# Kernel tuning notes

Measured on AMD Instinct MI355X. Metric: run time of the kernel, lower is better.

Reference implementation:

```python
import jax, jax.numpy as jnp
import numpy as np

N_HEAD = 16
SCALE = True


def setup_inputs() -> dict:
    key = jax.random.key(0)
    k1, k2, k3 = jax.random.split(key, 3)
    B, S, D = 4, 2048, 1024
    x = jax.random.normal(k1, (B, S, D), dtype=jnp.float32)
    w_attn = jax.random.normal(k2, (D, 3 * D), dtype=jnp.float32) * 0.02
    b_attn = jnp.zeros((3 * D,), dtype=jnp.float32)
    w_proj = jax.random.normal(k3, (D, D), dtype=jnp.float32) * 0.02
    b_proj = jnp.zeros((D,), dtype=jnp.float32)
    return {"x": x, "w_attn": w_attn, "b_attn": b_attn, "w_proj": w_proj, "b_proj": b_proj}


def reference(x, w_attn, b_attn, w_proj, b_proj):
    B, S, D = x.shape
    H = N_HEAD
    hd = D // H
    qkv = x @ w_attn + b_attn  # [B,S,3D] (Conv1D)
    q, k, v = jnp.split(qkv, 3, axis=-1)
    # split heads -> [B,H,S,hd]
    q = q.reshape(B, S, H, hd).transpose(0, 2, 1, 3)
    k = k.reshape(B, S, H, hd).transpose(0, 2, 1, 3)
    v = v.reshape(B, S, H, hd).transpose(0, 2, 1, 3)
    w = jnp.einsum('bhqd,bhkd->bhqk', q, k)  # [B,H,S,S]
    if SCALE:
        w = w / jnp.sqrt(jnp.asarray(hd, dtype=w.dtype))
    # causal mask exactly as in source: w*b + -10000*(1-b)
    bmask = jnp.tril(jnp.ones((S, S), dtype=w.dtype))[None, None]
    w = w * bmask + (-10000.0) * (1.0 - bmask)
    w = jax.nn.softmax(w, axis=-1)
    a = jnp.einsum('bhqk,bhkd->bhqd', w, v)  # [B,H,S,hd]
    a = a.transpose(0, 2, 1, 3).reshape(B, S, D)  # merge heads
    out = a @ w_proj + b_proj
    return out
```

## Files before the change

kernel.cpp:

```cpp
#include <hip/hip_runtime.h>

typedef __attribute__((ext_vector_type(8))) _Float16 f16x8;
typedef __attribute__((ext_vector_type(2))) __fp16 h16x2;
typedef __attribute__((ext_vector_type(4))) float f32x4;

#define S_LEN 2048
#define DMODEL 1024
#define NHEAD 16
#define HD 64
#define QKV_LD 3072
#define BTOT 4
#define LOG2E 1.4426950408889634f

#define GLL16(g, l)                                              \
  __builtin_amdgcn_global_load_lds(                              \
      (const __attribute__((address_space(1))) void*)(g),        \
      (__attribute__((address_space(3))) void*)(l), 16, 0, 0)

#define MFMA16(a, b, c) __builtin_amdgcn_mfma_f32_16x16x32_f16(a, b, c, 0, 0, 0)

__global__ __launch_bounds__(256) void cvt_f32_f16_k(const float* __restrict__ in,
                                                     _Float16* __restrict__ out, int n) {
  int i = (blockIdx.x * 256 + threadIdx.x) * 4;
  int stride = gridDim.x * 256 * 4;
  for (; i < n; i += stride) {
    float4 v = *(const float4*)(in + i);
    _Float16 h[4];
    h[0] = (_Float16)v.x; h[1] = (_Float16)v.y; h[2] = (_Float16)v.z; h[3] = (_Float16)v.w;
    *(uint2*)(out + i) = *(const uint2*)h;
  }
}

__global__ __launch_bounds__(256) void transpose_cvt_k(const float* __restrict__ W,
                                                       _Float16* __restrict__ Wt,
                                                       int K, int N) {
  __shared__ float t[32][33];
  int n0 = blockIdx.x * 32, k0 = blockIdx.y * 32;
  int tx = threadIdx.x, ty = threadIdx.y;
#pragma unroll
  for (int i = 0; i < 32; i += 8)
    t[ty + i][tx] = W[(size_t)(k0 + ty + i) * N + n0 + tx];
  __syncthreads();
#pragma unroll
  for (int i = 0; i < 32; i += 8)
    Wt[(size_t)(n0 + ty + i) * K + k0 + tx] = (_Float16)t[tx][ty + i];
}

template <int OUT_F32>
__global__ __launch_bounds__(256) void gemm_bt_k(const _Float16* __restrict__ A,
                                                 const _Float16* __restrict__ Bt,
                                                 const float* __restrict__ bias,
                                                 void* __restrict__ C,
                                                 int M, int N, int K) {
  __shared__ _Float16 As[128 * 64];
  __shared__ _Float16 Bs[128 * 64];
  const int tid = threadIdx.x;
  const int wid = tid >> 6, lane = tid & 63;
  const int quad = lane >> 4, l16 = lane & 15;
  const int wr = wid >> 1, wc = wid & 1;

  const int lin = blockIdx.y * gridDim.x + blockIdx.x;
  const int width = 8 * gridDim.x;
  const int group = lin / width;
  const int pm = group * 8 + (lin % width) % 8;
  const int pn = (lin % width) / 8;
  const int tm = pm * 128, tn = pn * 128;

  const int row0 = tid >> 3;
  const int xc = 8 * ((tid & 7) ^ (row0 & 7));
  const _Float16* Ag = A + (size_t)(tm + row0) * K + xc;
  const _Float16* Bg = Bt + (size_t)(tn + row0) * K + xc;
  _Float16* AsW = &As[wid * 512];
  _Float16* BsW = &Bs[wid * 512];

  f32x4 acc[4][4] = {};

  for (int k0 = 0; k0 < K; k0 += 64) {
    __syncthreads();
#pragma unroll
    for (int p = 0; p < 4; p++) {
      GLL16(Ag + k0 + (size_t)(32 * p) * K, AsW + 2048 * p);
      GLL16(Bg + k0 + (size_t)(32 * p) * K, BsW + 2048 * p);
    }
    __syncthreads();

#pragma unroll
    for (int ks = 0; ks < 2; ks++) {
      f16x8 af[4], bf[4];
#pragma unroll
      for (int mt = 0; mt < 4; mt++)
        af[mt] = *(const f16x8*)&As[(wr * 64 + mt * 16 + l16) * 64 +
                                    (((ks * 4 + quad) ^ (l16 & 7)) << 3)];
#pragma unroll
      for (int nt = 0; nt < 4; nt++)
        bf[nt] = *(const f16x8*)&Bs[(wc * 64 + nt * 16 + l16) * 64 +
                                    (((ks * 4 + quad) ^ (l16 & 7)) << 3)];
#pragma unroll
      for (int mt = 0; mt < 4; mt++)
#pragma unroll
        for (int nt = 0; nt < 4; nt++)
          acc[mt][nt] = MFMA16(af[mt], bf[nt], acc[mt][nt]);
    }
  }

#pragma unroll
  for (int nt = 0; nt < 4; nt++) {
    int col = tn + wc * 64 + nt * 16 + l16;
    float bv = bias[col];
#pragma unroll
    for (int mt = 0; mt < 4; mt++) {
      int row = tm + wr * 64 + mt * 16 + quad * 4;
#pragma unroll
      for (int r = 0; r < 4; r++) {
        float v = acc[mt][nt][r] + bv;
        if (OUT_F32)
          ((float*)C)[(size_t)(row + r) * N + col] = v;
        else
          ((_Float16*)C)[(size_t)(row + r) * N + col] = (_Float16)v;
      }
    }
  }
}

__global__ __launch_bounds__(512, 2) void gemm256_k(const _Float16* __restrict__ A,
                                                    const _Float16* __restrict__ Bt,
                                                    const float* __restrict__ bias,
                                                    _Float16* __restrict__ C,
                                                    int M, int N, int K) {
  __shared__ __align__(16) _Float16 sb[2][2][16384];
  const int tid = threadIdx.x;
  const int wid = tid >> 6, lane = tid & 63;
  const int quad = lane >> 4, l16 = lane & 15;
  const int wm = wid >> 2, wn = wid & 3;

  const int lin = blockIdx.y * gridDim.x + blockIdx.x;
  const int width = 8 * gridDim.x;
  const int group = lin / width;
  const int pm = group * 8 + (lin % width) % 8;
  const int pn = (lin % width) / 8;
  const int tm = pm * 256, tn = pn * 256;

  const int row0 = tid >> 3;
  const int xc = 8 * ((tid & 7) ^ (row0 & 7));
  const _Float16* Ag = A + (size_t)(tm + row0) * K + xc;
  const _Float16* Bg = Bt + (size_t)(tn + row0) * K + xc;

  f32x4 acc[8][4] = {};
  const int ntk = K >> 6;

  auto stage = [&](int t) {
    const int d = t & 1;
    const int k0 = t << 6;
#pragma unroll
    for (int r = 0; r < 4; r++) {
      GLL16(Ag + k0 + (size_t)(64 * r) * K, &sb[d][0][r * 4096 + wid * 512]);
      GLL16(Bg + k0 + (size_t)(64 * r) * K, &sb[d][1][r * 4096 + wid * 512]);
    }
  };

  stage(0);
  if (ntk > 1) stage(1);

  for (int t = 0; t < ntk; t++) {
    if (t + 1 < ntk)
      asm volatile("s_waitcnt vmcnt(8)" ::: "memory");
    else
      asm volatile("s_waitcnt vmcnt(0)" ::: "memory");
    __builtin_amdgcn_s_barrier();
    asm volatile("" ::: "memory");
    __builtin_amdgcn_sched_barrier(0);

    const _Float16* As_ = sb[t & 1][0];
    const _Float16* Bs_ = sb[t & 1][1];
    f16x8 bf[4][2];
#pragma unroll
    for (int n = 0; n < 4; n++)
#pragma unroll
      for (int ks = 0; ks < 2; ks++)
        bf[n][ks] = *(const f16x8*)&Bs_[(wn * 64 + n * 16 + l16) * 64 +
                                        (((ks * 4 + quad) ^ (l16 & 7)) << 3)];
#pragma unroll
    for (int mh = 0; mh < 2; mh++) {
      f16x8 af[4][2];
#pragma unroll
      for (int m = 0; m < 4; m++)
#pragma unroll
        for (int ks = 0; ks < 2; ks++)
          af[m][ks] =
              *(const f16x8*)&As_[(wm * 128 + mh * 64 + m * 16 + l16) * 64 +
                                  (((ks * 4 + quad) ^ (l16 & 7)) << 3)];
      __builtin_amdgcn_s_setprio(1);
#pragma unroll
      for (int ks = 0; ks < 2; ks++)
#pragma unroll
        for (int m = 0; m < 4; m++)
#pragma unroll
          for (int n = 0; n < 4; n++)
            acc[mh * 4 + m][n] = MFMA16(af[m][ks], bf[n][ks], acc[mh * 4 + m][n]);
      __builtin_amdgcn_s_setprio(0);
    }

    __builtin_amdgcn_s_barrier();
    asm volatile("" ::: "memory");
    __builtin_amdgcn_sched_barrier(0);
    if (t + 2 < ntk) stage(t + 2);
  }

#pragma unroll
  for (int n = 0; n < 4; n++) {
    int col = tn + wn * 64 + n * 16 + l16;
    float bv = bias[col];
#pragma unroll
    for (int m8 = 0; m8 < 8; m8++) {
      int row = tm + wm * 128 + m8 * 16 + quad * 4;
#pragma unroll
      for (int r = 0; r < 4; r++)
        C[(size_t)(row + r) * N + col] = (_Float16)(acc[m8][n][r] + bv);
    }
  }
}

__global__ __launch_bounds__(512, 4) void attn_k(const _Float16* __restrict__ qkv,
                                                 _Float16* __restrict__ out) {
  __shared__ __align__(16) char pool[53760];
  _Float16* KsB = (_Float16*)pool;
  _Float16* VTsB = (_Float16*)(pool + 16384);

  const int tid = threadIdx.x, wid = tid >> 6, lane = tid & 63;
  const int quad = lane >> 4, l16 = lane & 15;
  const int qg = wid & 3, kg = wid >> 2;
  _Float16* PsW = (_Float16*)(pool + 32768) + wid * 1280;
  const int bh = blockIdx.x, b = bh >> 4, h = bh & 15;
  const int p = blockIdx.y;
  const _Float16* base = qkv + (size_t)b * S_LEN * QKV_LD + h * HD;

  const int krow = tid >> 3;
  const _Float16* Kg = base + DMODEL + (size_t)krow * QKV_LD +
                       8 * ((tid & 7) ^ (krow & 7));
  const bool vstager = (tid < 256);
  const int kp = tid & 31, dbase = ((tid >> 5) & 7) * 8;
  const _Float16* Vg = base + 2 * DMODEL + (size_t)(2 * kp) * QKV_LD + dbase;

  int voff[8];
#pragma unroll
  for (int i = 0; i < 8; i++) {
    int d = dbase + i;
    voff[i] = d * 32 + (((kp >> 2) ^ (d & 7)) << 2) + (kp & 3);
  }

  auto stage_V = [&](int bufi, uint4 v0, uint4 v1) {
    union { uint4 u; _Float16 h[8]; } a, c;
    a.u = v0; c.u = v1;
    uint* VT32 = (uint*)(VTsB + bufi * 4096);
#pragma unroll
    for (int i = 0; i < 8; i++) {
      union { _Float16 h[2]; uint u; } w;
      w.h[0] = a.h[i]; w.h[1] = c.h[i];
      VT32[voff[i]] = w.u;
    }
  };

  auto run_pass = [&](int qt) {
    f16x8 bq[2][2];
    {
      const _Float16 qs = (_Float16)(0.125f * LOG2E);
#pragma unroll
      for (int nt = 0; nt < 2; nt++)
#pragma unroll
        for (int ks = 0; ks < 2; ks++) {
          union { uint4 u; f16x8 h; } v;
          v.u = *(const uint4*)(base +
                                (size_t)(qt + qg * 32 + nt * 16 + l16) * QKV_LD +
                                ks * 32 + quad * 8);
          bq[nt][ks] = v.h * qs;
        }
    }

    float l_i[2] = {0.f, 0.f};
    f32x4 o[4][2] = {};

    const int qmin_w = qt + qg * 32;
    const int qmax_w = qmin_w + 31;
    const int nj = qt / 64 + 2;

    __syncthreads();
    GLL16(Kg, KsB + wid * 512);
    if (vstager) stage_V(0, *(const uint4*)(Vg), *(const uint4*)(Vg + QKV_LD));
    __syncthreads();

    for (int j = 0; j < nj; j++) {
      const int cur = j & 1, nxt = cur ^ 1;
      const int k0g = j * 64;
      const bool pf = (j + 1 < nj);
      uint4 pv0, pv1;
      if (pf) {
        const int kn = k0g + 64;
        GLL16(Kg + (size_t)kn * QKV_LD, KsB + nxt * 4096 + wid * 512);
        if (vstager) {
          pv0 = *(const uint4*)(Vg + (size_t)kn * QKV_LD);
          pv1 = *(const uint4*)(Vg + (size_t)(kn + 1) * QKV_LD);
        }
      }

      const int kgbase = k0g + kg * 32;
      if (kgbase <= qmax_w) {
        const _Float16* Kc = KsB + cur * 4096;
        f32x4 sc[2][2];
#pragma unroll
        for (int mt = 0; mt < 2; mt++)
#pragma unroll
          for (int nt = 0; nt < 2; nt++)
            sc[mt][nt] = f32x4{-4.f, -4.f, -4.f, -4.f};
#pragma unroll
        for (int ks = 0; ks < 2; ks++)
#pragma unroll
          for (int mt = 0; mt < 2; mt++) {
            f16x8 ak = *(const f16x8*)&Kc[(kg * 32 + mt * 16 + l16) * 64 +
                                          (((ks * 4 + quad) ^ (l16 & 7)) << 3)];
            sc[mt][0] = MFMA16(ak, bq[0][ks], sc[mt][0]);
            sc[mt][1] = MFMA16(ak, bq[1][ks], sc[mt][1]);
          }

        const bool need_mask = (kgbase + 31 > qmin_w);
#pragma unroll
        for (int nt = 0; nt < 2; nt++) {
          const int qgl = qmin_w + nt * 16 + l16;
          float pe[8];
#pragma unroll
          for (int mt = 0; mt < 2; mt++)
#pragma unroll
            for (int r = 0; r < 4; r++) {
              float v = sc[mt][nt][r];
              if (need_mask) {
                int kgi = kgbase + mt * 16 + quad * 4 + r;
                v = (kgi <= qgl) ? v : -3.0e38f;
              }
              pe[mt * 4 + r] = __builtin_amdgcn_exp2f(v);
            }
          l_i[nt] += ((pe[0] + pe[1]) + (pe[2] + pe[3])) +
                     ((pe[4] + pe[5]) + (pe[6] + pe[7]));
#pragma unroll
          for (int mt = 0; mt < 2; mt++) {
            union { h16x2 h[2]; uint2 u; } w;
            w.h[0] = __builtin_amdgcn_cvt_pkrtz(pe[mt * 4 + 0], pe[mt * 4 + 1]);
            w.h[1] = __builtin_amdgcn_cvt_pkrtz(pe[mt * 4 + 2], pe[mt * 4 + 3]);
            *(uint2*)&PsW[(nt * 16 + l16) * 40 + mt * 16 + quad * 4] = w.u;
          }
        }

        const _Float16* Vc = VTsB + cur * 4096;
        f16x8 bp0 = *(const f16x8*)&PsW[l16 * 40 + quad * 8];
        f16x8 bp1 = *(const f16x8*)&PsW[(16 + l16) * 40 + quad * 8];
#pragma unroll
        for (int md = 0; md < 4; md++) {
          f16x8 av = *(const f16x8*)&Vc[(md * 16 + l16) * 64 +
                                        (((kg * 4 + quad) ^ (l16 & 7)) << 3)];
          o[md][0] = MFMA16(av, bp0, o[md][0]);
          o[md][1] = MFMA16(av, bp1, o[md][1]);
        }
      }

      if (pf && vstager) stage_V(nxt, pv0, pv1);
      __syncthreads();
    }

#pragma unroll
    for (int nt = 0; nt < 2; nt++) {
      float r = l_i[nt];
      r += __shfl_xor(r, 16, 64);
      r += __shfl_xor(r, 32, 64);
      l_i[nt] = r;
    }
    float* X = (float*)pool;
    float* ML = (float*)(pool + 53248);
    if (kg == 1) {
#pragma unroll
      for (int md = 0; md < 4; md++)
#pragma unroll
        for (int nt = 0; nt < 2; nt++)
          *(f32x4*)&X[qg * 2048 + (md * 2 + nt) * 256 + lane * 4] = o[md][nt];
      if (quad == 0) {
#pragma unroll
        for (int nt = 0; nt < 2; nt++)
          ML[(qg * 2 + nt) * 16 + l16] = l_i[nt];
      }
    }
    __syncthreads();
    if (kg == 0) {
      _Float16* PsE = (_Float16*)(pool + 32768) + qg * 2304;
      float inv[2];
#pragma unroll
      for (int nt = 0; nt < 2; nt++)
        inv[nt] = 1.0f / (l_i[nt] + ML[(qg * 2 + nt) * 16 + l16]);
#pragma unroll
      for (int md = 0; md < 4; md++)
#pragma unroll
        for (int nt = 0; nt < 2; nt++) {
          f32x4 o1 = *(const f32x4*)&X[qg * 2048 + (md * 2 + nt) * 256 + lane * 4];
          f32x4 ot = o[md][nt] + o1;
          union { h16x2 h[2]; uint2 u; } w;
          w.h[0] = __builtin_amdgcn_cvt_pkrtz(ot[0] * inv[nt], ot[1] * inv[nt]);
          w.h[1] = __builtin_amdgcn_cvt_pkrtz(ot[2] * inv[nt], ot[3] * inv[nt]);
          *(uint2*)&PsE[(nt * 16 + l16) * 72 + md * 16 + quad * 4] = w.u;
        }
      {
        int r = lane >> 1, ch = (lane & 1) * 32;
        const int qgl = qt + qg * 32 + r;
        _Float16* orow = out + (size_t)(b * S_LEN + qgl) * DMODEL + h * HD + ch;
#pragma unroll
        for (int i = 0; i < 4; i++)
          *(uint4*)(orow + i * 8) = *(const uint4*)&PsE[r * 72 + ch + i * 8];
      }
    }
  };

  run_pass(p * 128);
  run_pass((15 - p) * 128);
}

extern "C" void kernel_launch(void* const* d_in, const int* in_sizes, int n_in,
                              void* d_out, int out_size, void* d_ws, size_t ws_size,
                              hipStream_t stream) {
  const float* x = (const float*)d_in[0];
  const float* w_attn = (const float*)d_in[1];
  const float* b_attn = (const float*)d_in[2];
  const float* w_proj = (const float*)d_in[3];
  const float* b_proj = (const float*)d_in[4];
  float* outp = (float*)d_out;

  char* ws = (char*)d_ws;
  _Float16* x16 = (_Float16*)ws;
  _Float16* wTa = (_Float16*)(ws + 16777216);
  _Float16* wTp = (_Float16*)(ws + 16777216 + 6291456);
  _Float16* qkv = (_Float16*)(ws + 25165824);
  _Float16* abuf = (_Float16*)(ws + 75497472);

  const int nx = BTOT * S_LEN * DMODEL;

  cvt_f32_f16_k<<<8192, 256, 0, stream>>>(x, x16, nx);
  transpose_cvt_k<<<dim3(QKV_LD / 32, DMODEL / 32), dim3(32, 8), 0, stream>>>(
      w_attn, wTa, DMODEL, QKV_LD);
  transpose_cvt_k<<<dim3(DMODEL / 32, DMODEL / 32), dim3(32, 8), 0, stream>>>(
      w_proj, wTp, DMODEL, DMODEL);

  gemm256_k<<<dim3(QKV_LD / 256, BTOT * S_LEN / 256), 512, 0, stream>>>(
      x16, wTa, b_attn, qkv, BTOT * S_LEN, QKV_LD, DMODEL);

  attn_k<<<dim3(BTOT * NHEAD, 8), 512, 0, stream>>>(qkv, abuf);

  gemm_bt_k<1><<<dim3(DMODEL / 128, BTOT * S_LEN / 128), 256, 0, stream>>>(
      abuf, wTp, b_proj, outp, BTOT * S_LEN, DMODEL, DMODEL);
}
```

Baseline: 257.5 us.

## Interleave next-tile global loads across four MFMA phases in GEMM loop

Restructures the double-buffered GEMM main loop. Instead of prefetching two tiles ahead in one burst, it splits each K-tile into four compute phases and issues a quarter of the next tile's global-to-LDS loads before each phase, with barriers between phases. The goal is to spread memory traffic evenly under the MFMA work and keep fewer A/B fragments live in registers. In exchange, prefetch depth drops from two tiles to one and each iteration now carries more barriers and lgkmcnt waits.

```diff
diff --git a/kernel.cpp b/kernel.cpp
--- a/kernel.cpp
+++ b/kernel.cpp
@@ -148,62 +148,105 @@
   f32x4 acc[8][4] = {};
   const int ntk = K >> 6;
 
-  auto stage = [&](int t) {
-    const int d = t & 1;
-    const int k0 = t << 6;
-#pragma unroll
-    for (int r = 0; r < 4; r++) {
-      GLL16(Ag + k0 + (size_t)(64 * r) * K, &sb[d][0][r * 4096 + wid * 512]);
-      GLL16(Bg + k0 + (size_t)(64 * r) * K, &sb[d][1][r * 4096 + wid * 512]);
-    }
+  auto sA = [&](int t, int r) {
+    GLL16(Ag + (t << 6) + (size_t)(64 * r) * K, &sb[t & 1][0][r * 4096 + wid * 512]);
   };
-
-  stage(0);
-  if (ntk > 1) stage(1);
+  auto sB = [&](int t, int r) {
+    GLL16(Bg + (t << 6) + (size_t)(64 * r) * K, &sb[t & 1][1][r * 4096 + wid * 512]);
+  };
+
+#pragma unroll
+  for (int r = 0; r < 4; r++) { sA(0, r); sB(0, r); }
 
   for (int t = 0; t < ntk; t++) {
-    if (t + 1 < ntk)
-      asm volatile("s_waitcnt vmcnt(8)" ::: "memory");
-    else
-      asm volatile("s_waitcnt vmcnt(0)" ::: "memory");
-    __builtin_amdgcn_s_barrier();
-    asm volatile("" ::: "memory");
-    __builtin_amdgcn_sched_barrier(0);
-
     const _Float16* As_ = sb[t & 1][0];
     const _Float16* Bs_ = sb[t & 1][1];
-    f16x8 bf[4][2];
+    const bool pf = (t + 1 < ntk);
+    f16x8 bf[2][4];
+    f16x8 af[4];
+
+    if (pf) {
+      sA(t + 1, 0); sA(t + 1, 1);
+      asm volatile("s_waitcnt vmcnt(2)" ::: "memory");
+    } else {
+      asm volatile("s_waitcnt vmcnt(0)" ::: "memory");
+    }
+    __builtin_amdgcn_s_barrier();
+    __builtin_amdgcn_sched_barrier(0);
 #pragma unroll
     for (int n = 0; n < 4; n++)
-#pragma unroll
-      for (int ks = 0; ks < 2; ks++)
-        bf[n][ks] = *(const f16x8*)&Bs_[(wn * 64 + n * 16 + l16) * 64 +
-                                        (((ks * 4 + quad) ^ (l16 & 7)) << 3)];
-#pragma unroll
-    for (int mh = 0; mh < 2; mh++) {
-      f16x8 af[4][2];
-#pragma unroll
-      for (int m = 0; m < 4; m++)
-#pragma unroll
-        for (int ks = 0; ks < 2; ks++)
-          af[m][ks] =
-              *(const f16x8*)&As_[(wm * 128 + mh * 64 + m * 16 + l16) * 64 +
-                                  (((ks * 4 + quad) ^ (l16 & 7)) << 3)];
-      __builtin_amdgcn_s_setprio(1);
-#pragma unroll
-      for (int ks = 0; ks < 2; ks++)
-#pragma unroll
-        for (int m = 0; m < 4; m++)
-#pragma unroll
-          for (int n = 0; n < 4; n++)
-            acc[mh * 4 + m][n] = MFMA16(af[m][ks], bf[n][ks], acc[mh * 4 + m][n]);
-      __builtin_amdgcn_s_setprio(0);
-    }
-
+      bf[0][n] = *(const f16x8*)&Bs_[(wn * 64 + n * 16 + l16) * 64 +
+                                     ((quad ^ (l16 & 7)) << 3)];
+#pragma unroll
+    for (int m = 0; m < 4; m++)
+      af[m] = *(const f16x8*)&As_[(wm * 128 + m * 16 + l16) * 64 +
+                                  ((quad ^ (l16 & 7)) << 3)];
+    asm volatile("s_waitcnt lgkmcnt(0)" ::: "memory");
+    __builtin_amdgcn_sched_barrier(0);
+    __builtin_amdgcn_s_setprio(1);
+#pragma unroll
+    for (int m = 0; m < 4; m++)
+#pragma unroll
+      for (int n = 0; n < 4; n++)
+        acc[m][n] = MFMA16(af[m], bf[0][n], acc[m][n]);
+    __builtin_amdgcn_s_setprio(0);
     __builtin_amdgcn_s_barrier();
-    asm volatile("" ::: "memory");
-    __builtin_amdgcn_sched_barrier(0);
-    if (t + 2 < ntk) stage(t + 2);
+    __builtin_amdgcn_sched_barrier(0);
+
+    if (pf) { sA(t + 1, 2); sA(t + 1, 3); }
+#pragma unroll
+    for (int n = 0; n < 4; n++)
+      bf[1][n] = *(const f16x8*)&Bs_[(wn * 64 + n * 16 + l16) * 64 +
+                                     (((4 + quad) ^ (l16 & 7)) << 3)];
+#pragma unroll
+    for (int m = 0; m < 4; m++)
+      af[m] = *(const f16x8*)&As_[(wm * 128 + m * 16 + l16) * 64 +
+                                  (((4 + quad) ^ (l16 & 7)) << 3)];
+    asm volatile("s_waitcnt lgkmcnt(0)" ::: "memory");
+    __builtin_amdgcn_sched_barrier(0);
+    __builtin_amdgcn_s_setprio(1);
+#pragma unroll
+    for (int m = 0; m < 4; m++)
+#pragma unroll
+      for (int n = 0; n < 4; n++)
+        acc[m][n] = MFMA16(af[m], bf[1][n], acc[m][n]);
+    __builtin_amdgcn_s_setprio(0);
+    __builtin_amdgcn_s_barrier();
+    __builtin_amdgcn_sched_barrier(0);
+
+    if (pf) { sB(t + 1, 0); sB(t + 1, 1); }
+#pragma unroll
+    for (int m = 0; m < 4; m++)
+      af[m] = *(const f16x8*)&As_[(wm * 128 + 64 + m * 16 + l16) * 64 +
+                                  ((quad ^ (l16 & 7)) << 3)];
+    asm volatile("s_waitcnt lgkmcnt(0)" ::: "memory");
+    __builtin_amdgcn_sched_barrier(0);
+    __builtin_amdgcn_s_setprio(1);
+#pragma unroll
+    for (int m = 0; m < 4; m++)
+#pragma unroll
+      for (int n = 0; n < 4; n++)
+        acc[4 + m][n] = MFMA16(af[m], bf[0][n], acc[4 + m][n]);
+    __builtin_amdgcn_s_setprio(0);
+    __builtin_amdgcn_s_barrier();
+    __builtin_amdgcn_sched_barrier(0);
+
+    if (pf) { sB(t + 1, 2); sB(t + 1, 3); }
+#pragma unroll
+    for (int m = 0; m < 4; m++)
+      af[m] = *(const f16x8*)&As_[(wm * 128 + 64 + m * 16 + l16) * 64 +
+                                  (((4 + quad) ^ (l16 & 7)) << 3)];
+    asm volatile("s_waitcnt lgkmcnt(0)" ::: "memory");
+    __builtin_amdgcn_sched_barrier(0);
+    __builtin_amdgcn_s_setprio(1);
+#pragma unroll
+    for (int m = 0; m < 4; m++)
+#pragma unroll
+      for (int n = 0; n < 4; n++)
+        acc[4 + m][n] = MFMA16(af[m], bf[1][n], acc[4 + m][n]);
+    __builtin_amdgcn_s_setprio(0);
+    __builtin_amdgcn_s_barrier();
+    __builtin_amdgcn_sched_barrier(0);
   }
 
 #pragma unroll
```

Result: no change. 257.8 us (+0.1%).
